# Kernel tuning notes

Hardware: AMD Instinct MI355X
Metric: run time of the kernel (lower is better)

Reference implementation:

```python
import jax, jax.numpy as jnp
import numpy as np

N, H, W_SP, CIN = 32, 56, 56, 256
COUT, KH, KW = 256, 3, 3


def setup_inputs() -> dict:
    key = jax.random.key(0)
    k1, k2, k3 = jax.random.split(key, 3)
    x = jax.random.normal(k1, (N, H, W_SP, CIN), dtype=jnp.float32)
    W = jax.random.normal(k2, (KH, KW, CIN, COUT), dtype=jnp.float32) * 0.05
    b = jax.random.normal(k3, (COUT,), dtype=jnp.float32) * 0.05
    return {"x": x, "W": W, "b": b}


def reference(x, W, b):
    # Binarize weights to {-1, +1} via sign with straight-through estimator
    # (forward = sign(W), gradient = identity), matching tensorlayer's
    # binary_weight quantizer.
    bW = W + jax.lax.stop_gradient(jnp.sign(W) - W)
    # tf.nn.conv2d(x, bW, strides=(1,1,1,1), padding='SAME'), NHWC / HWIO
    y = jax.lax.conv_general_dilated(
        x, bW,
        window_strides=(1, 1),
        padding='SAME',
        dimension_numbers=('NHWC', 'HWIO', 'NHWC'),
    )
    y = y + b  # tf.nn.bias_add over channels
    return jax.nn.relu(y)
```

## Files before the change

### kernel.cpp

```cpp
#include <hip/hip_runtime.h>
#include <hip/hip_bf16.h>

#define CIN   256
#define COUT  256
#define HH    56
#define WW    56
#define NB    32
#define KTOT  2304
#define MTOT  (NB * HH * WW)

#define BM 128
#define BN 256
#define BK 64
#define NTHREADS 512
#define NSTEPS (KTOT / BK)

#define BT_BYTES  ((size_t)COUT * KTOT * 2)
#define XB_OFF    BT_BYTES
#define XB_BYTES  ((size_t)MTOT * CIN * 2)
#define ZB_OFF    (XB_OFF + XB_BYTES)
#define WS_NEEDED (ZB_OFF + 64)

typedef __attribute__((ext_vector_type(4))) float  f32x4;
typedef __attribute__((ext_vector_type(8))) __bf16 bf16x8;

__global__ void xcast_kernel(const float* __restrict__ x, __bf16* __restrict__ xb,
                             float* __restrict__ zbuf) {
    const size_t total = (size_t)MTOT * CIN / 8;
    size_t idx = (size_t)blockIdx.x * blockDim.x + threadIdx.x;
    const size_t stride = (size_t)gridDim.x * blockDim.x;
    for (size_t g = idx; g < total; g += stride) {
        f32x4 v0 = ((const f32x4*)x)[2 * g];
        f32x4 v1 = ((const f32x4*)x)[2 * g + 1];
        bf16x8 o;
        o[0] = (__bf16)v0[0]; o[1] = (__bf16)v0[1];
        o[2] = (__bf16)v0[2]; o[3] = (__bf16)v0[3];
        o[4] = (__bf16)v1[0]; o[5] = (__bf16)v1[1];
        o[6] = (__bf16)v1[2]; o[7] = (__bf16)v1[3];
        ((bf16x8*)xb)[g] = o;
    }
    if (blockIdx.x == 0 && threadIdx.x < 16) zbuf[threadIdx.x] = 0.f;
}

__global__ void binarize_w_kernel(const float* __restrict__ W,
                                  unsigned short* __restrict__ bt) {
    int k  = blockIdx.x;
    int co = threadIdx.x;
    int tap = k >> 8, cin = k & 255;
    int c = cin >> 6, ci = cin & 63;
    int ks = c * 9 + tap;
    float w = W[(size_t)k * COUT + co];
    unsigned short s = (w > 0.f) ? 0x3F80u : ((w < 0.f) ? 0xBF80u : 0u);
    bt[(size_t)co * KTOT + ks * 64 + (ci ^ ((co & 7) << 3))] = s;
}

__device__ __forceinline__ void gload_lds16(const void* g, void* l) {
    __builtin_amdgcn_global_load_lds(
        (const __attribute__((address_space(1))) void*)g,
        (__attribute__((address_space(3))) void*)l,
        16, 0, 0);
}

template<int USE_XB>
__global__ __launch_bounds__(NTHREADS, 4)
void bconv_kernel(const float* __restrict__ x,
                  const __bf16* __restrict__ xb,
                  const unsigned short* __restrict__ bt,
                  const float* __restrict__ bias,
                  float* __restrict__ out,
                  const char* __restrict__ zb) {
    __shared__ __bf16 Al[BM][BK];
    __shared__ __bf16 Bl[BN][BK];

    const int tid  = threadIdx.x;
    const int lane = tid & 63;
    const int wid  = tid >> 6;

    const int bid = blockIdx.x;
    const int swz = (bid & 7) * (MTOT / BM / 8) + (bid >> 3);
    const int m_base = swz * BM;

    const int wm = (wid & 1) * 64;
    const int wn = (wid >> 1) * 64;

    const int  rB0 = wid * 32 + (lane >> 3);
    const long bB0 = (long)rB0 * (KTOT * 2) + (lane & 7) * 16;

    int aH[2], aW[2], aOff[2];
    if (USE_XB) {
        const int chunk = (lane & 7) ^ ((lane >> 3) & 7);
#pragma unroll
        for (int i = 0; i < 2; ++i) {
            int r = (wid * 2 + i) * 8 + (lane >> 3);
            int flat = m_base + r;
            aW[i] = flat % WW;
            aH[i] = (flat / WW) % HH;
            aOff[i] = flat * (CIN * 2) + chunk * 16;
        }
    } else {
#pragma unroll
        for (int i = 0; i < 2; ++i) {
            int r = i * 64 + (tid >> 3);
            int flat = m_base + r;
            aW[i] = flat % WW;
            aH[i] = (flat / WW) % HH;
            aOff[i] = flat * (CIN * 4);
        }
    }

    f32x4 acc[4][4];
#pragma unroll
    for (int i = 0; i < 4; ++i)
#pragma unroll
        for (int j = 0; j < 4; ++j)
            acc[i][j] = (f32x4){0.f, 0.f, 0.f, 0.f};

    const char* xbb = (const char*)xb;
    const char* xfb = (const char*)x;
    const char* btb = (const char*)bt;

    for (int ks = 0; ks < NSTEPS; ++ks) {
        const int c    = ks / 9;
        const int tap  = ks % 9;
        const int dh   = tap / 3 - 1;
        const int dw   = tap % 3 - 1;
        const int doff = dh * WW + dw;

        __syncthreads();

#pragma unroll
        for (int i = 0; i < 4; ++i) {
            const char* g = btb + bB0 + (long)i * 8 * (KTOT * 2) + ks * 128;
            gload_lds16(g, &Bl[wid * 32 + i * 8][0]);
        }

        if (USE_XB) {
#pragma unroll
            for (int i = 0; i < 2; ++i) {
                int ih = aH[i] + dh, iw = aW[i] + dw;
                bool valid = ((unsigned)ih < (unsigned)HH) && ((unsigned)iw < (unsigned)WW);
                const char* g = valid ? (xbb + (long)(aOff[i] + doff * (CIN * 2) + c * 128))
                                      : zb;
                gload_lds16(g, &Al[(wid * 2 + i) * 8][0]);
            }
        } else {
            const int cg = tid & 7;
#pragma unroll
            for (int i = 0; i < 2; ++i) {
                int ih = aH[i] + dh, iw = aW[i] + dw;
                f32x4 v0 = (f32x4){0.f, 0.f, 0.f, 0.f};
                f32x4 v1 = (f32x4){0.f, 0.f, 0.f, 0.f};
                if (((unsigned)ih < (unsigned)HH) && ((unsigned)iw < (unsigned)WW)) {
                    const float* gp = (const float*)(xfb +
                        (long)(aOff[i] + doff * (CIN * 4) + c * 256 + cg * 32));
                    v0 = ((const f32x4*)gp)[0];
                    v1 = ((const f32x4*)gp)[1];
                }
                bf16x8 o;
                o[0] = (__bf16)v0[0]; o[1] = (__bf16)v0[1];
                o[2] = (__bf16)v0[2]; o[3] = (__bf16)v0[3];
                o[4] = (__bf16)v1[0]; o[5] = (__bf16)v1[1];
                o[6] = (__bf16)v1[2]; o[7] = (__bf16)v1[3];
                int r = i * 64 + (tid >> 3);
                *(bf16x8*)((char*)&Al[0][0] + r * 128 + ((cg * 16) ^ ((r & 7) << 4))) = o;
            }
        }

        __syncthreads();

        const char* Ab = (const char*)&Al[0][0];
        const char* Bb = (const char*)&Bl[0][0];
        const int swzr = (lane & 7) << 4;
        const int rsel = lane & 15;
        const int csel = (lane >> 4) * 16;
#pragma unroll
        for (int kk = 0; kk < 2; ++kk) {
            const int colb = kk * 64 + csel;
            bf16x8 af[4], bfr[4];
#pragma unroll
            for (int mi = 0; mi < 4; ++mi)
                af[mi] = *(const bf16x8*)(Ab + (wm + mi * 16 + rsel) * 128 + (colb ^ swzr));
#pragma unroll
            for (int ni = 0; ni < 4; ++ni)
                bfr[ni] = *(const bf16x8*)(Bb + (wn + ni * 16 + rsel) * 128 + (colb ^ swzr));
#pragma unroll
            for (int mi = 0; mi < 4; ++mi)
#pragma unroll
                for (int ni = 0; ni < 4; ++ni)
                    acc[mi][ni] = __builtin_amdgcn_mfma_f32_16x16x32_bf16(
                        af[mi], bfr[ni], acc[mi][ni], 0, 0, 0);
        }
    }

    const int col_l  = lane & 15;
    const int row_g4 = (lane >> 4) * 4;
#pragma unroll
    for (int ni = 0; ni < 4; ++ni) {
        const int cout = wn + ni * 16 + col_l;
        const float bv = bias[cout];
#pragma unroll
        for (int mi = 0; mi < 4; ++mi) {
            const int row = m_base + wm + mi * 16 + row_g4;
#pragma unroll
            for (int j = 0; j < 4; ++j) {
                float v = acc[mi][ni][j] + bv;
                out[(size_t)(row + j) * COUT + cout] = v > 0.f ? v : 0.f;
            }
        }
    }
}

extern "C" void kernel_launch(void* const* d_in, const int* in_sizes, int n_in,
                              void* d_out, int out_size, void* d_ws, size_t ws_size,
                              hipStream_t stream) {
    const float* x = (const float*)d_in[0];
    const float* W = (const float*)d_in[1];
    const float* b = (const float*)d_in[2];
    float* out = (float*)d_out;

    char* ws = (char*)d_ws;
    unsigned short* bt = (unsigned short*)ws;
    __bf16* xb   = (__bf16*)(ws + XB_OFF);
    float*  zbuf = (float*)(ws + ZB_OFF);

    const bool use_xb = (ws_size >= WS_NEEDED);

    binarize_w_kernel<<<dim3(KTOT), dim3(COUT), 0, stream>>>(W, bt);
    if (use_xb) {
        xcast_kernel<<<dim3(2048), dim3(256), 0, stream>>>(x, xb, zbuf);
        bconv_kernel<1><<<dim3(MTOT / BM), dim3(NTHREADS), 0, stream>>>(
            x, xb, bt, b, out, (const char*)zbuf);
    } else {
        bconv_kernel<0><<<dim3(MTOT / BM), dim3(NTHREADS), 0, stream>>>(
            x, xb, bt, b, out, nullptr);
    }
}
```

Before: 151.5 us.

## Double-buffer LDS with BK=32 and 4-wave 128x256 tiles in bconv

```diff
diff --git a/kernel.cpp b/kernel.cpp
--- a/kernel.cpp
+++ b/kernel.cpp
@@ -11,8 +11,8 @@
 
 #define BM 128
 #define BN 256
-#define BK 64
-#define NTHREADS 512
+#define BK 32
+#define NTHREADS 256
 #define NSTEPS (KTOT / BK)
 
 #define BT_BYTES  ((size_t)COUT * KTOT * 2)
@@ -23,6 +23,13 @@
 
 typedef __attribute__((ext_vector_type(4))) float  f32x4;
 typedef __attribute__((ext_vector_type(8))) __bf16 bf16x8;
+
+__device__ __forceinline__ void gload_lds16(const void* g, void* l) {
+    __builtin_amdgcn_global_load_lds(
+        (const __attribute__((address_space(1))) void*)g,
+        (__attribute__((address_space(3))) void*)l,
+        16, 0, 0);
+}
 
 __global__ void xcast_kernel(const float* __restrict__ x, __bf16* __restrict__ xb,
                              float* __restrict__ zbuf) {
@@ -47,6 +54,138 @@
     int k  = blockIdx.x;
     int co = threadIdx.x;
     int tap = k >> 8, cin = k & 255;
+    int c2 = cin >> 5, ci = cin & 31;
+    int ks = c2 * 9 + tap;
+    float w = W[(size_t)k * COUT + co];
+    unsigned short s = (w > 0.f) ? 0x3F80u : ((w < 0.f) ? 0xBF80u : 0u);
+    bt[(size_t)co * KTOT + ks * 32 + (ci ^ ((co & 3) << 3))] = s;
+}
+
+__global__ __launch_bounds__(NTHREADS, 2)
+void bconv_kernel(const __bf16* __restrict__ xb,
+                  const unsigned short* __restrict__ bt,
+                  const float* __restrict__ bias,
+                  float* __restrict__ out,
+                  const char* __restrict__ zb) {
+    __shared__ __bf16 Al[2][BM][BK];
+    __shared__ __bf16 Bl[2][BN][BK];
+
+    const int tid  = threadIdx.x;
+    const int lane = tid & 63;
+    const int wid  = tid >> 6;
+
+    const int bid = blockIdx.x;
+    const int swz = (bid & 7) * (MTOT / BM / 8) + (bid >> 3);
+    const int m_base = swz * BM;
+
+    const int wn = wid * 64;
+
+    const int    rB  = wid * 16 + (lane >> 2);
+    const size_t bB0 = (size_t)rB * (KTOT * 2) + (size_t)(lane & 3) * 16;
+
+    const int chunk = (lane & 3) ^ ((lane >> 2) & 3);
+    int aH[2], aW[2];
+    long aOff[2];
+#pragma unroll
+    for (int i = 0; i < 2; ++i) {
+        int r = i * 64 + wid * 16 + (lane >> 2);
+        int flat = m_base + r;
+        aW[i] = flat % WW;
+        aH[i] = (flat / WW) % HH;
+        aOff[i] = (long)flat * (CIN * 2) + chunk * 16;
+    }
+
+    f32x4 acc[8][4];
+#pragma unroll
+    for (int i = 0; i < 8; ++i)
+#pragma unroll
+        for (int j = 0; j < 4; ++j)
+            acc[i][j] = (f32x4){0.f, 0.f, 0.f, 0.f};
+
+    const char* xbb = (const char*)xb;
+    const char* btb = (const char*)bt;
+
+    auto STAGE = [&](int ks, int buf) {
+#pragma unroll
+        for (int j = 0; j < 4; ++j)
+            gload_lds16(btb + bB0 + (size_t)j * 64 * (KTOT * 2) + (size_t)ks * 64,
+                        &Bl[buf][j * 64 + wid * 16][0]);
+        const int c2  = ks / 9;
+        const int tap = ks - c2 * 9;
+        const int dh  = tap / 3 - 1;
+        const int dw  = tap % 3 - 1;
+        const int doff = dh * WW + dw;
+#pragma unroll
+        for (int i = 0; i < 2; ++i) {
+            int ih = aH[i] + dh, iw = aW[i] + dw;
+            bool valid = ((unsigned)ih < (unsigned)HH) && ((unsigned)iw < (unsigned)WW);
+            const char* g = valid ? (xbb + aOff[i] + (long)doff * (CIN * 2) + c2 * 64)
+                                  : (const char*)zb;
+            gload_lds16(g, &Al[buf][i * 64 + wid * 16][0]);
+        }
+    };
+
+    STAGE(0, 0);
+
+    const int rsel = lane & 15;
+    const int cb   = (lane >> 4) * 16;
+    const int sw   = (lane & 3) << 4;
+
+    for (int ks = 0; ks < NSTEPS; ++ks) {
+        const int cur = ks & 1;
+        if (ks + 1 < NSTEPS) {
+            STAGE(ks + 1, cur ^ 1);
+            asm volatile("s_waitcnt vmcnt(6)" ::: "memory");
+        } else {
+            asm volatile("s_waitcnt vmcnt(0)" ::: "memory");
+        }
+        __builtin_amdgcn_s_barrier();
+        asm volatile("" ::: "memory");
+
+        const char* Ab = (const char*)&Al[cur][0][0];
+        const char* Bb = (const char*)&Bl[cur][0][0];
+        bf16x8 af[8], bfr[4];
+#pragma unroll
+        for (int ni = 0; ni < 4; ++ni)
+            bfr[ni] = *(const bf16x8*)(Bb + (wn + ni * 16 + rsel) * (BK * 2) + (cb ^ sw));
+#pragma unroll
+        for (int mi = 0; mi < 8; ++mi)
+            af[mi] = *(const bf16x8*)(Ab + (mi * 16 + rsel) * (BK * 2) + (cb ^ sw));
+#pragma unroll
+        for (int mi = 0; mi < 8; ++mi)
+#pragma unroll
+            for (int ni = 0; ni < 4; ++ni)
+                acc[mi][ni] = __builtin_amdgcn_mfma_f32_16x16x32_bf16(
+                    af[mi], bfr[ni], acc[mi][ni], 0, 0, 0);
+
+        asm volatile("s_waitcnt lgkmcnt(0)" ::: "memory");
+        __builtin_amdgcn_s_barrier();
+        asm volatile("" ::: "memory");
+    }
+
+    const int col_l  = lane & 15;
+    const int row_g4 = (lane >> 4) * 4;
+#pragma unroll
+    for (int ni = 0; ni < 4; ++ni) {
+        const int cout = wn + ni * 16 + col_l;
+        const float bv = bias[cout];
+#pragma unroll
+        for (int mi = 0; mi < 8; ++mi) {
+            const int row = m_base + mi * 16 + row_g4;
+#pragma unroll
+            for (int j = 0; j < 4; ++j) {
+                float v = acc[mi][ni][j] + bv;
+                out[(size_t)(row + j) * COUT + cout] = v > 0.f ? v : 0.f;
+            }
+        }
+    }
+}
+
+__global__ void binarize_w_old_kernel(const float* __restrict__ W,
+                                      unsigned short* __restrict__ bt) {
+    int k  = blockIdx.x;
+    int co = threadIdx.x;
+    int tap = k >> 8, cin = k & 255;
     int c = cin >> 6, ci = cin & 63;
     int ks = c * 9 + tap;
     float w = W[(size_t)k * COUT + co];
@@ -54,31 +193,21 @@
     bt[(size_t)co * KTOT + ks * 64 + (ci ^ ((co & 7) << 3))] = s;
 }
 
-__device__ __forceinline__ void gload_lds16(const void* g, void* l) {
-    __builtin_amdgcn_global_load_lds(
-        (const __attribute__((address_space(1))) void*)g,
-        (__attribute__((address_space(3))) void*)l,
-        16, 0, 0);
-}
-
-template<int USE_XB>
-__global__ __launch_bounds__(NTHREADS, 4)
-void bconv_kernel(const float* __restrict__ x,
-                  const __bf16* __restrict__ xb,
-                  const unsigned short* __restrict__ bt,
-                  const float* __restrict__ bias,
-                  float* __restrict__ out,
-                  const char* __restrict__ zb) {
-    __shared__ __bf16 Al[BM][BK];
-    __shared__ __bf16 Bl[BN][BK];
+__global__ __launch_bounds__(512, 4)
+void bconv_old_kernel(const float* __restrict__ x,
+                      const unsigned short* __restrict__ bt,
+                      const float* __restrict__ bias,
+                      float* __restrict__ out) {
+    __shared__ __bf16 Al[128][64];
+    __shared__ __bf16 Bl[256][64];
 
     const int tid  = threadIdx.x;
     const int lane = tid & 63;
     const int wid  = tid >> 6;
 
     const int bid = blockIdx.x;
-    const int swz = (bid & 7) * (MTOT / BM / 8) + (bid >> 3);
-    const int m_base = swz * BM;
+    const int swz = (bid & 7) * (MTOT / 128 / 8) + (bid >> 3);
+    const int m_base = swz * 128;
 
     const int wm = (wid & 1) * 64;
     const int wn = (wid >> 1) * 64;
@@ -87,25 +216,13 @@
     const long bB0 = (long)rB0 * (KTOT * 2) + (lane & 7) * 16;
 
     int aH[2], aW[2], aOff[2];
-    if (USE_XB) {
-        const int chunk = (lane & 7) ^ ((lane >> 3) & 7);
-#pragma unroll
-        for (int i = 0; i < 2; ++i) {
-            int r = (wid * 2 + i) * 8 + (lane >> 3);
-            int flat = m_base + r;
-            aW[i] = flat % WW;
-            aH[i] = (flat / WW) % HH;
-            aOff[i] = flat * (CIN * 2) + chunk * 16;
-        }
-    } else {
-#pragma unroll
-        for (int i = 0; i < 2; ++i) {
-            int r = i * 64 + (tid >> 3);
-            int flat = m_base + r;
-            aW[i] = flat % WW;
-            aH[i] = (flat / WW) % HH;
-            aOff[i] = flat * (CIN * 4);
-        }
+#pragma unroll
+    for (int i = 0; i < 2; ++i) {
+        int r = i * 64 + (tid >> 3);
+        int flat = m_base + r;
+        aW[i] = flat % WW;
+        aH[i] = (flat / WW) % HH;
+        aOff[i] = flat * (CIN * 4);
     }
 
     f32x4 acc[4][4];
@@ -115,11 +232,10 @@
         for (int j = 0; j < 4; ++j)
             acc[i][j] = (f32x4){0.f, 0.f, 0.f, 0.f};
 
-    const char* xbb = (const char*)xb;
     const char* xfb = (const char*)x;
     const char* btb = (const char*)bt;
 
-    for (int ks = 0; ks < NSTEPS; ++ks) {
+    for (int ks = 0; ks < 36; ++ks) {
         const int c    = ks / 9;
         const int tap  = ks % 9;
         const int dh   = tap / 3 - 1;
@@ -134,36 +250,25 @@
             gload_lds16(g, &Bl[wid * 32 + i * 8][0]);
         }
 
-        if (USE_XB) {
-#pragma unroll
-            for (int i = 0; i < 2; ++i) {
-                int ih = aH[i] + dh, iw = aW[i] + dw;
-                bool valid = ((unsigned)ih < (unsigned)HH) && ((unsigned)iw < (unsigned)WW);
-                const char* g = valid ? (xbb + (long)(aOff[i] + doff * (CIN * 2) + c * 128))
-                                      : zb;
-                gload_lds16(g, &Al[(wid * 2 + i) * 8][0]);
+        const int cg = tid & 7;
+#pragma unroll
+        for (int i = 0; i < 2; ++i) {
+            int ih = aH[i] + dh, iw = aW[i] + dw;
+            f32x4 v0 = (f32x4){0.f, 0.f, 0.f, 0.f};
+            f32x4 v1 = (f32x4){0.f, 0.f, 0.f, 0.f};
+            if (((unsigned)ih < (unsigned)HH) && ((unsigned)iw < (unsigned)WW)) {
+                const float* gp = (const float*)(xfb +
+                    (long)(aOff[i] + doff * (CIN * 4) + c * 256 + cg * 32));
+                v0 = ((const f32x4*)gp)[0];
+                v1 = ((const f32x4*)gp)[1];
             }
-        } else {
-            const int cg = tid & 7;
-#pragma unroll
-            for (int i = 0; i < 2; ++i) {
-                int ih = aH[i] + dh, iw = aW[i] + dw;
-                f32x4 v0 = (f32x4){0.f, 0.f, 0.f, 0.f};
-                f32x4 v1 = (f32x4){0.f, 0.f, 0.f, 0.f};
-                if (((unsigned)ih < (unsigned)HH) && ((unsigned)iw < (unsigned)WW)) {
-                    const float* gp = (const float*)(xfb +
-                        (long)(aOff[i] + doff * (CIN * 4) + c * 256 + cg * 32));
-                    v0 = ((const f32x4*)gp)[0];
-                    v1 = ((const f32x4*)gp)[1];
-                }
-                bf16x8 o;
-                o[0] = (__bf16)v0[0]; o[1] = (__bf16)v0[1];
-                o[2] = (__bf16)v0[2]; o[3] = (__bf16)v0[3];
-                o[4] = (__bf16)v1[0]; o[5] = (__bf16)v1[1];
-                o[6] = (__bf16)v1[2]; o[7] = (__bf16)v1[3];
-                int r = i * 64 + (tid >> 3);
-                *(bf16x8*)((char*)&Al[0][0] + r * 128 + ((cg * 16) ^ ((r & 7) << 4))) = o;
-            }
+            bf16x8 o;
+            o[0] = (__bf16)v0[0]; o[1] = (__bf16)v0[1];
+            o[2] = (__bf16)v0[2]; o[3] = (__bf16)v0[3];
+            o[4] = (__bf16)v1[0]; o[5] = (__bf16)v1[1];
+            o[6] = (__bf16)v1[2]; o[7] = (__bf16)v1[3];
+            int r = i * 64 + (tid >> 3);
+            *(bf16x8*)((char*)&Al[0][0] + r * 128 + ((cg * 16) ^ ((r & 7) << 4))) = o;
         }
 
         __syncthreads();
@@ -223,15 +328,13 @@
     __bf16* xb   = (__bf16*)(ws + XB_OFF);
     float*  zbuf = (float*)(ws + ZB_OFF);
 
-    const bool use_xb = (ws_size >= WS_NEEDED);
-
-    binarize_w_kernel<<<dim3(KTOT), dim3(COUT), 0, stream>>>(W, bt);
-    if (use_xb) {
+    if (ws_size >= WS_NEEDED) {
+        binarize_w_kernel<<<dim3(KTOT), dim3(COUT), 0, stream>>>(W, bt);
         xcast_kernel<<<dim3(2048), dim3(256), 0, stream>>>(x, xb, zbuf);
-        bconv_kernel<1><<<dim3(MTOT / BM), dim3(NTHREADS), 0, stream>>>(
-            x, xb, bt, b, out, (const char*)zbuf);
+        bconv_kernel<<<dim3(MTOT / BM), dim3(NTHREADS), 0, stream>>>(
+            xb, bt, b, out, (const char*)zbuf);
     } else {
-        bconv_kernel<0><<<dim3(MTOT / BM), dim3(NTHREADS), 0, stream>>>(
-            x, xb, bt, b, out, nullptr);
-    }
-}
+        binarize_w_old_kernel<<<dim3(KTOT), dim3(COUT), 0, stream>>>(W, bt);
+        bconv_old_kernel<<<dim3(MTOT / 128), dim3(512), 0, stream>>>(x, bt, b, out);
+    }
+}
```

Result: slower. 188.1 us (+24.2%).
